# Performance work log

Hardware: AMD Instinct MI355X
Metric: run time of the kernel (lower is better)

Reference implementation:

```python
import jax, jax.numpy as jnp
import numpy as np

N, D, F1, F2, F3, H = 4096, 512, 64, 32, 16, 4
ALPHA = 0.2  # LeakyReLU negative slope
NEG = -9e15


def setup_inputs() -> dict:
    key = jax.random.key(0)
    ks = jax.random.split(key, 11)
    # sparse binary adjacency with self loops (adj.to_dense() in original)
    adj = (jax.random.uniform(ks[1], (N, N)) < 0.01).astype(jnp.float32)
    adj = jnp.maximum(adj, jnp.eye(N, dtype=jnp.float32))
    return {
        "x": jax.random.normal(ks[0], (N, D), jnp.float32),
        "adj": adj,
        "W_heads": jax.random.normal(ks[2], (H, D, F1), jnp.float32) * 0.05,
        "a_heads": jax.random.normal(ks[3], (H, 2 * F1, 1), jnp.float32) * 0.05,
        "W_att": jax.random.normal(ks[4], (H * F1, F1), jnp.float32) * 0.05,
        "a_att": jax.random.normal(ks[5], (2 * F1, 1), jnp.float32) * 0.05,
        "W1": jax.random.normal(ks[6], (F1, F2), jnp.float32) * 0.05,
        "W2": jax.random.normal(ks[7], (F2, F3), jnp.float32) * 0.05,
        "W3": jax.random.normal(ks[8], (F2, F3), jnp.float32) * 0.05,
        "eps": jax.random.normal(ks[9], (N, F3), jnp.float32),
    }


def _gat(x, adj, W, a, out_dim):
    Wh = x @ W                                   # [N, F]
    e = (Wh @ a[:out_dim]) + (Wh @ a[out_dim:]).T  # [N,1] + [1,N] -> [N,N]
    e = jax.nn.leaky_relu(e, negative_slope=ALPHA)
    att = jax.nn.softmax(jnp.where(adj > 0, e, NEG), axis=-1)
    return jax.nn.elu(att @ Wh)                  # [N, F]


def reference(x, adj, W_heads, a_heads, W_att, a_att, W1, W2, W3, eps):
    # multi-head GAT, concat along feature dim
    heads = jax.vmap(lambda W, a: _gat(x, adj, W, a, F1))(W_heads, a_heads)  # [H,N,F1]
    cat = jnp.transpose(heads, (1, 0, 2)).reshape(N, H * F1)
    gc_att = _gat(cat, adj, W_att, a_att, F1)    # [N, F1]
    # GCN layers (dropout off, no bias): spmm(adj, x @ W)
    h1 = jax.nn.relu(adj @ (gc_att @ W1))        # [N, F2]
    mu = adj @ (h1 @ W2)                         # [N, F3]
    logvar = adj @ (h1 @ W3)                     # [N, F3]
    # reparameterize (vae_bool=True): eps * exp(logvar) + mu
    z = eps * jnp.exp(logvar) + mu
    adj_rec = z @ z.T                            # inner-product decoder [N,N]
    return adj_rec, mu, logvar
```

## Files before the change

kernel.cpp:

```cpp
#include <hip/hip_runtime.h>
#include <math.h>

#define NN 4096
#define DD 512
#define F1 64
#define F2 32
#define F3 16
#define NH 4
#define ALPHA 0.2f
#define CAP 160
#define KS 4

__device__ __forceinline__ float lrelu(float e) { return (e >= 0.f) ? e : ALPHA * e; }

__global__ void k_csr(const float* __restrict__ adj, int* __restrict__ colidx,
                      int* __restrict__ deg) {
  __shared__ int cnt;
  int i = blockIdx.x, tid = threadIdx.x;
  if (tid == 0) cnt = 0;
  __syncthreads();
  const float4* arow = (const float4*)(adj + (size_t)i * NN);
  for (int t = tid; t < NN / 4; t += 256) {
    float4 v = arow[t];
    int base = t * 4;
    if (v.x != 0.f) { int p = atomicAdd(&cnt, 1); if (p < CAP) colidx[(size_t)i * CAP + p] = base; }
    if (v.y != 0.f) { int p = atomicAdd(&cnt, 1); if (p < CAP) colidx[(size_t)i * CAP + p] = base + 1; }
    if (v.z != 0.f) { int p = atomicAdd(&cnt, 1); if (p < CAP) colidx[(size_t)i * CAP + p] = base + 2; }
    if (v.w != 0.f) { int p = atomicAdd(&cnt, 1); if (p < CAP) colidx[(size_t)i * CAP + p] = base + 3; }
  }
  __syncthreads();
  if (tid == 0) deg[i] = cnt < CAP ? cnt : CAP;
}

__global__ __launch_bounds__(256, 4) void k_wh_gemm(
    const float* __restrict__ x, const float* __restrict__ W_heads,
    float* __restrict__ part) {
  __shared__ float As[32][65];
  __shared__ float Bs[32][64];
  int tid = threadIdx.x;
  int h = blockIdx.y;
  int r0 = blockIdx.x * 64;
  int kq = blockIdx.z;
  const float* Wh = W_heads + (size_t)h * DD * F1 + (size_t)kq * 128 * F1;

  int sr = tid >> 3, sq = tid & 7;
  int bk = tid >> 4, bf = tid & 15;
  int rg = tid >> 4, cg = tid & 15;

  const float* xa0 = x + (size_t)(r0 + sr) * DD + kq * 128;
  const float* xa1 = x + (size_t)(r0 + sr + 32) * DD + kq * 128;

  float4 pa0 = *(const float4*)(xa0 + sq * 4);
  float4 pa1 = *(const float4*)(xa1 + sq * 4);
  float4 pb0 = *(const float4*)(Wh + (size_t)bk * F1 + bf * 4);
  float4 pb1 = *(const float4*)(Wh + (size_t)(bk + 16) * F1 + bf * 4);

  float acc[4][4] = {};
  for (int c = 0; c < 4; ++c) {
    __syncthreads();
    {
      float* a0p = &As[sq * 4][sr];
      a0p[0] = pa0.x; a0p[65] = pa0.y; a0p[130] = pa0.z; a0p[195] = pa0.w;
      float* a1p = &As[sq * 4][sr + 32];
      a1p[0] = pa1.x; a1p[65] = pa1.y; a1p[130] = pa1.z; a1p[195] = pa1.w;
      *(float4*)&Bs[bk][bf * 4] = pb0;
      *(float4*)&Bs[bk + 16][bf * 4] = pb1;
    }
    __syncthreads();
    if (c < 3) {
      int k0 = (c + 1) * 32;
      pa0 = *(const float4*)(xa0 + k0 + sq * 4);
      pa1 = *(const float4*)(xa1 + k0 + sq * 4);
      pb0 = *(const float4*)(Wh + (size_t)(k0 + bk) * F1 + bf * 4);
      pb1 = *(const float4*)(Wh + (size_t)(k0 + bk + 16) * F1 + bf * 4);
    }
#pragma unroll
    for (int kk = 0; kk < 32; ++kk) {
      float4 av = *(const float4*)&As[kk][rg * 4];
      float4 bv = *(const float4*)&Bs[kk][cg * 4];
      acc[0][0] = fmaf(av.x, bv.x, acc[0][0]);
      acc[0][1] = fmaf(av.x, bv.y, acc[0][1]);
      acc[0][2] = fmaf(av.x, bv.z, acc[0][2]);
      acc[0][3] = fmaf(av.x, bv.w, acc[0][3]);
      acc[1][0] = fmaf(av.y, bv.x, acc[1][0]);
      acc[1][1] = fmaf(av.y, bv.y, acc[1][1]);
      acc[1][2] = fmaf(av.y, bv.z, acc[1][2]);
      acc[1][3] = fmaf(av.y, bv.w, acc[1][3]);
      acc[2][0] = fmaf(av.z, bv.x, acc[2][0]);
      acc[2][1] = fmaf(av.z, bv.y, acc[2][1]);
      acc[2][2] = fmaf(av.z, bv.z, acc[2][2]);
      acc[2][3] = fmaf(av.z, bv.w, acc[2][3]);
      acc[3][0] = fmaf(av.w, bv.x, acc[3][0]);
      acc[3][1] = fmaf(av.w, bv.y, acc[3][1]);
      acc[3][2] = fmaf(av.w, bv.z, acc[3][2]);
      acc[3][3] = fmaf(av.w, bv.w, acc[3][3]);
    }
  }

  float* dst = part + (size_t)kq * NN * (NH * F1);
#pragma unroll
  for (int r = 0; r < 4; ++r) {
    int row = r0 + rg * 4 + r;
    *(float4*)&dst[(size_t)row * (NH * F1) + h * 64 + cg * 4] =
        make_float4(acc[r][0], acc[r][1], acc[r][2], acc[r][3]);
  }
}

__global__ void k_wh_comb(const float* __restrict__ part,
                          const float* __restrict__ a_heads,
                          float* __restrict__ Whcat,
                          float* __restrict__ s1, float* __restrict__ s2) {
  int tid = threadIdx.x;
  int r0 = blockIdx.x * 8;
  int h = tid >> 6, f = tid & 63;
  float a1 = a_heads[h * 2 * F1 + f];
  float a2 = a_heads[h * 2 * F1 + F1 + f];
  const size_t stride = (size_t)NN * (NH * F1);
#pragma unroll
  for (int r = 0; r < 8; ++r) {
    size_t off = (size_t)(r0 + r) * (NH * F1) + tid;
    float v = part[off] + part[off + stride] + part[off + 2 * stride] +
              part[off + 3 * stride];
    Whcat[off] = v;
    float v1 = v * a1, v2 = v * a2;
#pragma unroll
    for (int o = 32; o > 0; o >>= 1) {
      v1 += __shfl_down(v1, o, 64);
      v2 += __shfl_down(v2, o, 64);
    }
    if (f == 0) {
      s1[h * NN + r0 + r] = v1;
      s2[h * NN + r0 + r] = v2;
    }
  }
}

__global__ void k_gat_heads(const int* __restrict__ colidx, const int* __restrict__ deg,
                            const float* __restrict__ Whcat,
                            const float* __restrict__ s1, const float* __restrict__ s2,
                            float* __restrict__ cat) {
  __shared__ int idx[CAP];
  __shared__ float wsh[NH][CAP];
  int i = blockIdx.x, tid = threadIdx.x;
  int c = deg[i];
  for (int t = tid; t < c; t += 256) idx[t] = colidx[(size_t)i * CAP + t];
  __syncthreads();
  int h = tid >> 6;
  int f = tid & 63;
  const float* s2h = s2 + h * NN;
  float s1v = s1[h * NN + i];
  float M = -INFINITY;
  for (int k = f; k < c; k += 64) {
    float v = s2h[idx[k]];
    wsh[h][k] = v;
    M = fmaxf(M, v);
  }
#pragma unroll
  for (int off = 32; off > 0; off >>= 1) M = fmaxf(M, __shfl_down(M, off, 64));
  M = __shfl(M, 0, 64);
  float m = lrelu(s1v + M);
  float lsum = 0.f;
  for (int k = f; k < c; k += 64) {
    float w = __expf(lrelu(s1v + wsh[h][k]) - m);
    wsh[h][k] = w;
    lsum += w;
  }
#pragma unroll
  for (int off = 32; off > 0; off >>= 1) lsum += __shfl_down(lsum, off, 64);
  float linv = 1.f / __shfl(lsum, 0, 64);
  __syncthreads();
  const float* base = Whcat + h * 64 + f;
  float a0 = 0.f, a1 = 0.f, a2 = 0.f, a3 = 0.f;
  int k = 0;
  for (; k + 4 <= c; k += 4) {
    int j0 = idx[k], j1 = idx[k + 1], j2 = idx[k + 2], j3 = idx[k + 3];
    a0 = fmaf(wsh[h][k],     base[(size_t)j0 * 256], a0);
    a1 = fmaf(wsh[h][k + 1], base[(size_t)j1 * 256], a1);
    a2 = fmaf(wsh[h][k + 2], base[(size_t)j2 * 256], a2);
    a3 = fmaf(wsh[h][k + 3], base[(size_t)j3 * 256], a3);
  }
  for (; k < c; ++k) a0 = fmaf(wsh[h][k], base[(size_t)idx[k] * 256], a0);
  float o = (a0 + a1 + a2 + a3) * linv;
  cat[(size_t)i * (NH * F1) + tid] = (o > 0.f) ? o : expm1f(o);
}

__global__ void k_wh2(const float* __restrict__ cat,
                      const float* __restrict__ W_att,
                      const float* __restrict__ a_att,
                      float* __restrict__ Wh2,
                      float* __restrict__ s1b, float* __restrict__ s2b) {
  const int ROWS = 8;
  __shared__ float cs[ROWS][NH * F1];
  int tid = threadIdx.x;
  int r0 = blockIdx.x * ROWS;
  const float4* csrc = (const float4*)(cat + (size_t)r0 * 256);
  for (int t = tid; t < ROWS * 256 / 4; t += 256) ((float4*)cs)[t] = csrc[t];
  __syncthreads();
  int g = tid >> 6;
  int f = tid & 63;
  float a1 = a_att[f], a2 = a_att[64 + f];
  const float* W = W_att + f;
#pragma unroll
  for (int rr = 0; rr < 2; ++rr) {
    int r = g * 2 + rr;
    float acc = 0.f;
    for (int k = 0; k < 256; k += 4) {
      float4 cv = *(const float4*)&cs[r][k];
      acc = fmaf(cv.x, W[(k + 0) * 64], acc);
      acc = fmaf(cv.y, W[(k + 1) * 64], acc);
      acc = fmaf(cv.z, W[(k + 2) * 64], acc);
      acc = fmaf(cv.w, W[(k + 3) * 64], acc);
    }
    Wh2[(size_t)(r0 + r) * 64 + f] = acc;
    float v1 = acc * a1, v2 = acc * a2;
#pragma unroll
    for (int off = 32; off > 0; off >>= 1) {
      v1 += __shfl_down(v1, off, 64);
      v2 += __shfl_down(v2, off, 64);
    }
    if (f == 0) { s1b[r0 + r] = v1; s2b[r0 + r] = v2; }
  }
}

__global__ void k_gat2t1(const int* __restrict__ colidx, const int* __restrict__ deg,
                         const float* __restrict__ Wh2,
                         const float* __restrict__ s1b, const float* __restrict__ s2b,
                         const float* __restrict__ W1, float* __restrict__ t1) {
  __shared__ int idx4[4][CAP];
  __shared__ float wsh4[4][CAP];
  __shared__ float grow[4][64];
  __shared__ float W1s[F1 * F2];
  int tid = threadIdx.x;
  int w = tid >> 6, f = tid & 63;
  int i = blockIdx.x * 4 + w;
  int c = deg[i];
  for (int t = tid; t < F1 * F2; t += 256) W1s[t] = W1[t];
  for (int k = f; k < c; k += 64) idx4[w][k] = colidx[(size_t)i * CAP + k];
  __syncthreads();
  float s1v = s1b[i];
  float M = -INFINITY;
  for (int k = f; k < c; k += 64) {
    float v = s2b[idx4[w][k]];
    wsh4[w][k] = v;
    M = fmaxf(M, v);
  }
#pragma unroll
  for (int off = 32; off > 0; off >>= 1) M = fmaxf(M, __shfl_down(M, off, 64));
  M = __shfl(M, 0, 64);
  float m = lrelu(s1v + M);
  float lsum = 0.f;
  for (int k = f; k < c; k += 64) {
    float wv = __expf(lrelu(s1v + wsh4[w][k]) - m);
    wsh4[w][k] = wv;
    lsum += wv;
  }
#pragma unroll
  for (int off = 32; off > 0; off >>= 1) lsum += __shfl_down(lsum, off, 64);
  float linv = 1.f / __shfl(lsum, 0, 64);
  __syncthreads();
  const float* base = Wh2 + f;
  float a0 = 0.f, a1 = 0.f, a2 = 0.f, a3 = 0.f;
  int k = 0;
  for (; k + 4 <= c; k += 4) {
    int j0 = idx4[w][k], j1 = idx4[w][k + 1], j2 = idx4[w][k + 2], j3 = idx4[w][k + 3];
    a0 = fmaf(wsh4[w][k],     base[(size_t)j0 * 64], a0);
    a1 = fmaf(wsh4[w][k + 1], base[(size_t)j1 * 64], a1);
    a2 = fmaf(wsh4[w][k + 2], base[(size_t)j2 * 64], a2);
    a3 = fmaf(wsh4[w][k + 3], base[(size_t)j3 * 64], a3);
  }
  for (; k < c; ++k) a0 = fmaf(wsh4[w][k], base[(size_t)idx4[w][k] * 64], a0);
  float o = (a0 + a1 + a2 + a3) * linv;
  grow[w][f] = (o > 0.f) ? o : expm1f(o);
  __syncthreads();
  if (f < F2) {
    float acc = 0.f;
#pragma unroll 8
    for (int kk = 0; kk < F1; ++kk) acc = fmaf(grow[w][kk], W1s[kk * F2 + f], acc);
    t1[(size_t)i * F2 + f] = acc;
  }
}

__global__ void k_gcn1t23(const int* __restrict__ colidx, const int* __restrict__ deg,
                          const float* __restrict__ t1,
                          const float* __restrict__ W2, const float* __restrict__ W3,
                          float* __restrict__ t23) {
  __shared__ int idx4[4][CAP];
  __shared__ float hrow[4][F2];
  __shared__ float Wc[F2 * 32];
  int tid = threadIdx.x;
  int w = tid >> 6, lane = tid & 63;
  int nb = lane >> 5, g = lane & 31;
  int i = blockIdx.x * 4 + w;
  int c = deg[i];
  for (int t = tid; t < F2 * 32; t += 256) {
    int kk = t >> 5, gg = t & 31;
    Wc[t] = (gg < 16) ? W2[kk * 16 + gg] : W3[kk * 16 + (gg - 16)];
  }
  for (int k = lane; k < c; k += 64) idx4[w][k] = colidx[(size_t)i * CAP + k];
  __syncthreads();
  float a0 = 0.f, a1 = 0.f;
  int k = nb;
  for (; k + 2 < c; k += 4) {
    a0 += t1[(size_t)idx4[w][k] * F2 + g];
    a1 += t1[(size_t)idx4[w][k + 2] * F2 + g];
  }
  for (; k < c; k += 2) a0 += t1[(size_t)idx4[w][k] * F2 + g];
  float tot = a0 + a1;
  tot += __shfl_xor(tot, 32, 64);
  float h1v = fmaxf(tot, 0.f);
  if (nb == 0) hrow[w][g] = h1v;
  __syncthreads();
  if (lane < 32) {
    float acc = 0.f;
#pragma unroll 8
    for (int kk = 0; kk < F2; ++kk) acc = fmaf(hrow[w][kk], Wc[kk * 32 + lane], acc);
    t23[(size_t)i * 32 + lane] = acc;
  }
}

__global__ void k_gcn2(const int* __restrict__ colidx, const int* __restrict__ deg,
                       const float* __restrict__ t23, const float* __restrict__ eps,
                       float* __restrict__ mu_out, float* __restrict__ lv_out,
                       float* __restrict__ z) {
  __shared__ int idx4[4][CAP];
  int tid = threadIdx.x;
  int w = tid >> 6, lane = tid & 63;
  int nb = lane >> 5, g = lane & 31;
  int i = blockIdx.x * 4 + w;
  int c = deg[i];
  for (int k = lane; k < c; k += 64) idx4[w][k] = colidx[(size_t)i * CAP + k];
  __syncthreads();
  float a0 = 0.f, a1 = 0.f;
  int k = nb;
  for (; k + 2 < c; k += 4) {
    a0 += t23[(size_t)idx4[w][k] * 32 + g];
    a1 += t23[(size_t)idx4[w][k + 2] * 32 + g];
  }
  for (; k < c; k += 2) a0 += t23[(size_t)idx4[w][k] * 32 + g];
  float tot = a0 + a1;
  tot += __shfl_xor(tot, 32, 64);
  float lvv = __shfl(tot, (lane & 31) + 16, 64);
  if (lane < 16) {
    mu_out[(size_t)i * 16 + g] = tot;
    z[(size_t)i * 16 + g] = eps[(size_t)i * 16 + g] * expf(lvv) + tot;
  } else if (lane < 32) {
    lv_out[(size_t)i * 16 + (g - 16)] = tot;
  }
}

__global__ void k_zzt(const float* __restrict__ z, float* __restrict__ out) {
  __shared__ float zr[64][17];
  __shared__ float zc[64][17];
  int bj = blockIdx.x, bi = blockIdx.y;
  int tid = threadIdx.x;
  for (int t = tid; t < 64 * 16; t += 256) {
    int r = t >> 4, kk = t & 15;
    zr[r][kk] = z[(size_t)(bi * 64 + r) * 16 + kk];
    zc[r][kk] = z[(size_t)(bj * 64 + r) * 16 + kk];
  }
  __syncthreads();
  int rg = tid >> 4;
  int cg = tid & 15;
  float acc[4][4] = {};
  for (int kk = 0; kk < 16; ++kk) {
    float av[4], bv[4];
#pragma unroll
    for (int t = 0; t < 4; ++t) av[t] = zr[rg * 4 + t][kk];
#pragma unroll
    for (int t = 0; t < 4; ++t) bv[t] = zc[cg * 4 + t][kk];
#pragma unroll
    for (int r = 0; r < 4; ++r)
#pragma unroll
      for (int cc = 0; cc < 4; ++cc) acc[r][cc] = fmaf(av[r], bv[cc], acc[r][cc]);
  }
#pragma unroll
  for (int r = 0; r < 4; ++r) {
    float4 v = make_float4(acc[r][0], acc[r][1], acc[r][2], acc[r][3]);
    *(float4*)&out[(size_t)(bi * 64 + rg * 4 + r) * NN + bj * 64 + cg * 4] = v;
  }
}

extern "C" void kernel_launch(void* const* d_in, const int* in_sizes, int n_in,
                              void* d_out, int out_size, void* d_ws, size_t ws_size,
                              hipStream_t stream) {
  const float* x       = (const float*)d_in[0];
  const float* adj     = (const float*)d_in[1];
  const float* W_heads = (const float*)d_in[2];
  const float* a_heads = (const float*)d_in[3];
  const float* W_att   = (const float*)d_in[4];
  const float* a_att   = (const float*)d_in[5];
  const float* W1      = (const float*)d_in[6];
  const float* W2      = (const float*)d_in[7];
  const float* W3      = (const float*)d_in[8];
  const float* eps     = (const float*)d_in[9];

  float* out = (float*)d_out;
  float* adj_rec = out;
  float* mu_out  = out + (size_t)NN * NN;
  float* lv_out  = mu_out + (size_t)NN * F3;

  float* ws = (float*)d_ws;
  float* Whcat = ws;               ws += (size_t)NN * NH * F1;
  float* s1    = ws;               ws += (size_t)NH * NN;
  float* s2    = ws;               ws += (size_t)NH * NN;
  float* cat   = ws;               ws += (size_t)NN * NH * F1;
  float* Wh2   = ws;               ws += (size_t)NN * F1;
  float* s1b   = ws;               ws += NN;
  float* s2b   = ws;               ws += NN;
  float* t1    = ws;               ws += (size_t)NN * F2;
  float* t23   = ws;               ws += (size_t)NN * 2 * F3;
  float* z     = ws;               ws += (size_t)NN * F3;
  int*   colidx = (int*)ws;        ws += (size_t)NN * CAP;
  int*   deg    = (int*)ws;        ws += NN;
  float* part  = (float*)ws;       ws += (size_t)KS * NN * NH * F1;

  k_csr<<<NN, 256, 0, stream>>>(adj, colidx, deg);
  k_wh_gemm<<<dim3(64, NH, KS), 256, 0, stream>>>(x, W_heads, part);
  k_wh_comb<<<NN / 8, 256, 0, stream>>>(part, a_heads, Whcat, s1, s2);
  k_gat_heads<<<NN, 256, 0, stream>>>(colidx, deg, Whcat, s1, s2, cat);
  k_wh2<<<NN / 8, 256, 0, stream>>>(cat, W_att, a_att, Wh2, s1b, s2b);
  k_gat2t1<<<NN / 4, 256, 0, stream>>>(colidx, deg, Wh2, s1b, s2b, W1, t1);
  k_gcn1t23<<<NN / 4, 256, 0, stream>>>(colidx, deg, t1, W2, W3, t23);
  k_gcn2<<<NN / 4, 256, 0, stream>>>(colidx, deg, t23, eps, mu_out, lv_out, z);
  k_zzt<<<dim3(64, 64), 256, 0, stream>>>(z, adj_rec);
}
```

Baseline: 224.7 us.

## Enlarge x@W_heads GEMM tiles to 128x128 with 8x8 per-thread microtiles

Reworks the multi-head projection GEMM so each block computes a 128-row by 128-column tile covering two heads, with an 8x8 register microtile per thread, and splits K into 8 chunks of 64 instead of 4 chunks of 128. The aim is more FMA work per shared-memory load and better operand reuse. The combine kernel is vectorised with float4 to sum 8 partials and reduces the attention dot products over 16-lane groups. In exchange, register pressure rises, the launch-bounds occupancy hint is dropped, and the partial buffer doubles, so the combine step moves more memory.

```diff
diff --git a/kernel.cpp b/kernel.cpp
--- a/kernel.cpp
+++ b/kernel.cpp
@@ -9,7 +9,7 @@
 #define NH 4
 #define ALPHA 0.2f
 #define CAP 160
-#define KS 4
+#define KS 8
 
 __device__ __forceinline__ float lrelu(float e) { return (e >= 0.f) ? e : ALPHA * e; }
 
@@ -32,78 +32,81 @@
   if (tid == 0) deg[i] = cnt < CAP ? cnt : CAP;
 }
 
-__global__ __launch_bounds__(256, 4) void k_wh_gemm(
+__global__ __launch_bounds__(256) void k_wh_gemm(
     const float* __restrict__ x, const float* __restrict__ W_heads,
     float* __restrict__ part) {
-  __shared__ float As[32][65];
-  __shared__ float Bs[32][64];
-  int tid = threadIdx.x;
-  int h = blockIdx.y;
-  int r0 = blockIdx.x * 64;
-  int kq = blockIdx.z;
-  const float* Wh = W_heads + (size_t)h * DD * F1 + (size_t)kq * 128 * F1;
-
-  int sr = tid >> 3, sq = tid & 7;
-  int bk = tid >> 4, bf = tid & 15;
+  __shared__ float As[32][128];
+  __shared__ float Bs[32][128];
+  int tid = threadIdx.x;
+  int nh = blockIdx.y;
+  int r0 = blockIdx.x * 128;
+  int kb = blockIdx.z * 64;
+
+  int arow = tid & 127, ahalf = tid >> 7;
+  int bk = tid >> 5, bf = tid & 31;
   int rg = tid >> 4, cg = tid & 15;
 
-  const float* xa0 = x + (size_t)(r0 + sr) * DD + kq * 128;
-  const float* xa1 = x + (size_t)(r0 + sr + 32) * DD + kq * 128;
-
-  float4 pa0 = *(const float4*)(xa0 + sq * 4);
-  float4 pa1 = *(const float4*)(xa1 + sq * 4);
-  float4 pb0 = *(const float4*)(Wh + (size_t)bk * F1 + bf * 4);
-  float4 pb1 = *(const float4*)(Wh + (size_t)(bk + 16) * F1 + bf * 4);
-
-  float acc[4][4] = {};
-  for (int c = 0; c < 4; ++c) {
+  const float* xa = x + (size_t)(r0 + arow) * DD + kb + ahalf * 16;
+  int h = nh * 2 + (bf >> 4);
+  const float* wsrc = W_heads + (size_t)h * DD * F1 + ((bf * 4) & 63);
+
+  float4 a_pre[4], b_pre[4];
+#pragma unroll
+  for (int q = 0; q < 4; ++q) a_pre[q] = *(const float4*)(xa + q * 4);
+#pragma unroll
+  for (int q = 0; q < 4; ++q)
+    b_pre[q] = *(const float4*)(wsrc + (size_t)(kb + bk + q * 8) * F1);
+
+  float acc[8][8] = {};
+#pragma unroll
+  for (int c = 0; c < 2; ++c) {
+#pragma unroll
+    for (int q = 0; q < 4; ++q) {
+      int kk = ahalf * 16 + q * 4;
+      As[kk + 0][arow] = a_pre[q].x;
+      As[kk + 1][arow] = a_pre[q].y;
+      As[kk + 2][arow] = a_pre[q].z;
+      As[kk + 3][arow] = a_pre[q].w;
+    }
+#pragma unroll
+    for (int q = 0; q < 4; ++q)
+      *(float4*)&Bs[bk + q * 8][bf * 4] = b_pre[q];
     __syncthreads();
-    {
-      float* a0p = &As[sq * 4][sr];
-      a0p[0] = pa0.x; a0p[65] = pa0.y; a0p[130] = pa0.z; a0p[195] = pa0.w;
-      float* a1p = &As[sq * 4][sr + 32];
-      a1p[0] = pa1.x; a1p[65] = pa1.y; a1p[130] = pa1.z; a1p[195] = pa1.w;
-      *(float4*)&Bs[bk][bf * 4] = pb0;
-      *(float4*)&Bs[bk + 16][bf * 4] = pb1;
-    }
-    __syncthreads();
-    if (c < 3) {
-      int k0 = (c + 1) * 32;
-      pa0 = *(const float4*)(xa0 + k0 + sq * 4);
-      pa1 = *(const float4*)(xa1 + k0 + sq * 4);
-      pb0 = *(const float4*)(Wh + (size_t)(k0 + bk) * F1 + bf * 4);
-      pb1 = *(const float4*)(Wh + (size_t)(k0 + bk + 16) * F1 + bf * 4);
+    if (c == 0) {
+#pragma unroll
+      for (int q = 0; q < 4; ++q) a_pre[q] = *(const float4*)(xa + 32 + q * 4);
+#pragma unroll
+      for (int q = 0; q < 4; ++q)
+        b_pre[q] = *(const float4*)(wsrc + (size_t)(kb + 32 + bk + q * 8) * F1);
     }
 #pragma unroll
     for (int kk = 0; kk < 32; ++kk) {
-      float4 av = *(const float4*)&As[kk][rg * 4];
-      float4 bv = *(const float4*)&Bs[kk][cg * 4];
-      acc[0][0] = fmaf(av.x, bv.x, acc[0][0]);
-      acc[0][1] = fmaf(av.x, bv.y, acc[0][1]);
-      acc[0][2] = fmaf(av.x, bv.z, acc[0][2]);
-      acc[0][3] = fmaf(av.x, bv.w, acc[0][3]);
-      acc[1][0] = fmaf(av.y, bv.x, acc[1][0]);
-      acc[1][1] = fmaf(av.y, bv.y, acc[1][1]);
-      acc[1][2] = fmaf(av.y, bv.z, acc[1][2]);
-      acc[1][3] = fmaf(av.y, bv.w, acc[1][3]);
-      acc[2][0] = fmaf(av.z, bv.x, acc[2][0]);
-      acc[2][1] = fmaf(av.z, bv.y, acc[2][1]);
-      acc[2][2] = fmaf(av.z, bv.z, acc[2][2]);
-      acc[2][3] = fmaf(av.z, bv.w, acc[2][3]);
-      acc[3][0] = fmaf(av.w, bv.x, acc[3][0]);
-      acc[3][1] = fmaf(av.w, bv.y, acc[3][1]);
-      acc[3][2] = fmaf(av.w, bv.z, acc[3][2]);
-      acc[3][3] = fmaf(av.w, bv.w, acc[3][3]);
-    }
-  }
-
-  float* dst = part + (size_t)kq * NN * (NH * F1);
-#pragma unroll
-  for (int r = 0; r < 4; ++r) {
-    int row = r0 + rg * 4 + r;
-    *(float4*)&dst[(size_t)row * (NH * F1) + h * 64 + cg * 4] =
-        make_float4(acc[r][0], acc[r][1], acc[r][2], acc[r][3]);
-  }
+      float ar[8], bc[8];
+      *(float4*)&ar[0] = *(const float4*)&As[kk][rg * 4];
+      *(float4*)&ar[4] = *(const float4*)&As[kk][rg * 4 + 64];
+      *(float4*)&bc[0] = *(const float4*)&Bs[kk][cg * 4];
+      *(float4*)&bc[4] = *(const float4*)&Bs[kk][cg * 4 + 64];
+#pragma unroll
+      for (int r = 0; r < 8; ++r)
+#pragma unroll
+        for (int cc = 0; cc < 8; ++cc)
+          acc[r][cc] = fmaf(ar[r], bc[cc], acc[r][cc]);
+    }
+    if (c == 0) __syncthreads();
+  }
+
+  float* dst = part + (size_t)blockIdx.z * NN * (NH * F1) + nh * 128;
+#pragma unroll
+  for (int rh = 0; rh < 2; ++rh)
+#pragma unroll
+    for (int r = 0; r < 4; ++r) {
+      int row = r0 + rh * 64 + rg * 4 + r;
+      float* p = dst + (size_t)row * (NH * F1);
+      *(float4*)&p[cg * 4] = make_float4(acc[rh * 4 + r][0], acc[rh * 4 + r][1],
+                                         acc[rh * 4 + r][2], acc[rh * 4 + r][3]);
+      *(float4*)&p[cg * 4 + 64] = make_float4(acc[rh * 4 + r][4], acc[rh * 4 + r][5],
+                                              acc[rh * 4 + r][6], acc[rh * 4 + r][7]);
+    }
 }
 
 __global__ void k_wh_comb(const float* __restrict__ part,
@@ -112,25 +115,34 @@
                           float* __restrict__ s1, float* __restrict__ s2) {
   int tid = threadIdx.x;
   int r0 = blockIdx.x * 8;
-  int h = tid >> 6, f = tid & 63;
-  float a1 = a_heads[h * 2 * F1 + f];
-  float a2 = a_heads[h * 2 * F1 + F1 + f];
+  int rb = tid >> 6;
+  int c4 = tid & 63;
+  int h = c4 >> 4;
+  int f0 = (c4 & 15) * 4;
+  float4 a1 = *(const float4*)&a_heads[h * 2 * F1 + f0];
+  float4 a2 = *(const float4*)&a_heads[h * 2 * F1 + F1 + f0];
   const size_t stride = (size_t)NN * (NH * F1);
 #pragma unroll
-  for (int r = 0; r < 8; ++r) {
-    size_t off = (size_t)(r0 + r) * (NH * F1) + tid;
-    float v = part[off] + part[off + stride] + part[off + 2 * stride] +
-              part[off + 3 * stride];
-    Whcat[off] = v;
-    float v1 = v * a1, v2 = v * a2;
-#pragma unroll
-    for (int o = 32; o > 0; o >>= 1) {
-      v1 += __shfl_down(v1, o, 64);
-      v2 += __shfl_down(v2, o, 64);
-    }
-    if (f == 0) {
-      s1[h * NN + r0 + r] = v1;
-      s2[h * NN + r0 + r] = v2;
+  for (int rr = 0; rr < 2; ++rr) {
+    int row = r0 + rb * 2 + rr;
+    size_t off = (size_t)row * (NH * F1) + c4 * 4;
+    float4 v = *(const float4*)&part[off];
+#pragma unroll
+    for (int s = 1; s < KS; ++s) {
+      float4 p = *(const float4*)&part[off + (size_t)s * stride];
+      v.x += p.x; v.y += p.y; v.z += p.z; v.w += p.w;
+    }
+    *(float4*)&Whcat[off] = v;
+    float v1 = v.x * a1.x + v.y * a1.y + v.z * a1.z + v.w * a1.w;
+    float v2 = v.x * a2.x + v.y * a2.y + v.z * a2.z + v.w * a2.w;
+#pragma unroll
+    for (int o = 8; o > 0; o >>= 1) {
+      v1 += __shfl_down(v1, o, 16);
+      v2 += __shfl_down(v2, o, 16);
+    }
+    if ((tid & 15) == 0) {
+      s1[h * NN + row] = v1;
+      s2[h * NN + row] = v2;
     }
   }
 }
@@ -415,7 +427,7 @@
   float* part  = (float*)ws;       ws += (size_t)KS * NN * NH * F1;
 
   k_csr<<<NN, 256, 0, stream>>>(adj, colidx, deg);
-  k_wh_gemm<<<dim3(64, NH, KS), 256, 0, stream>>>(x, W_heads, part);
+  k_wh_gemm<<<dim3(32, 2, KS), 256, 0, stream>>>(x, W_heads, part);
   k_wh_comb<<<NN / 8, 256, 0, stream>>>(part, a_heads, Whcat, s1, s2);
   k_gat_heads<<<NN, 256, 0, stream>>>(colidx, deg, Whcat, s1, s2, cat);
   k_wh2<<<NN / 8, 256, 0, stream>>>(cat, W_att, a_att, Wh2, s1b, s2b);
```

New measurement: 224.4 us. No clear change (-0.1%).
